# Kernel optimization log

Measured on AMD Instinct MI355X. Metric: run time of the kernel, lower is better.

## Reference

```python
import jax, jax.numpy as jnp
import numpy as np

L, H, C, V, BLK = 6, 16, 1024, 32000, 2048
B, T, TA = 2, 512, 512
DFF = 4 * C
STD = 0.02
PROJ_STD = 0.02 / np.sqrt(2 * L)  # c_proj init per module
SCALE = 1.0 / np.sqrt(C // H)


def setup_inputs() -> dict:
    key = jax.random.key(0)
    ks = iter(jax.random.split(key, 64))
    nrm = lambda shape, std=STD: jax.random.normal(next(ks), shape, jnp.float32) * std
    inp = {
        'idx': jax.random.randint(next(ks), (B, T), 0, V),
        'xa': jax.random.normal(next(ks), (B, TA, C), jnp.float32),
        'wte': nrm((V, C)),            # tied with lm_head
        'wpe': nrm((BLK, C)),
        'ln1_w': jnp.ones((L, C)), 'ln1_b': jnp.zeros((L, C)),
        'sa_wq': nrm((L, C, C)), 'sa_bq': jnp.zeros((L, C)),
        'sa_wk': nrm((L, C, C)), 'sa_bk': jnp.zeros((L, C)),
        'sa_wv': nrm((L, C, C)), 'sa_bv': jnp.zeros((L, C)),
        'sa_wo': nrm((L, C, C), PROJ_STD), 'sa_bo': jnp.zeros((L, C)),
        'ca_wq': nrm((L, C, C)), 'ca_bq': jnp.zeros((L, C)),
        'ca_wk': nrm((L, C, C)), 'ca_bk': jnp.zeros((L, C)),
        'ca_wv': nrm((L, C, C)), 'ca_bv': jnp.zeros((L, C)),
        'ca_wo': nrm((L, C, C), PROJ_STD), 'ca_bo': jnp.zeros((L, C)),
        'ln2_w': jnp.ones((L, C)), 'ln2_b': jnp.zeros((L, C)),
        'fc_w': nrm((L, C, DFF)), 'fc_b': jnp.zeros((L, DFF)),
        'pr_w': nrm((L, DFF, C), PROJ_STD), 'pr_b': jnp.zeros((L, C)),
        'lnf_w': jnp.ones((C,)), 'lnf_b': jnp.zeros((C,)),
    }
    return inp


def _ln(h, w, b):
    m = h.mean(-1, keepdims=True)
    v = jnp.mean((h - m) ** 2, -1, keepdims=True)
    return (h - m) * jax.lax.rsqrt(v + 1e-5) * w + b


def _gelu(h):  # new_gelu (tanh approximation)
    return 0.5 * h * (1.0 + jnp.tanh(np.sqrt(2.0 / np.pi) * (h + 0.044715 * h ** 3)))


def _attn(hq, hkv, wq, bq, wk, bk, wv, bv, wo, bo):
    # NB: the original applies a tril causal mask even for cross-attention.
    Bq, Tq, _ = hq.shape
    Tk = hkv.shape[1]
    D = C // H
    q = (hq @ wq + bq).reshape(Bq, Tq, H, D)
    k = (hkv @ wk + bk).reshape(Bq, Tk, H, D)
    v = (hkv @ wv + bv).reshape(Bq, Tk, H, D)
    att = jnp.einsum('bqhd,bkhd->bhqk', q, k) * SCALE
    mask = jnp.tril(jnp.ones((Tq, Tk), bool))
    att = jnp.where(mask, att, -jnp.inf)
    att = jax.nn.softmax(att, axis=-1)
    y = jnp.einsum('bhqk,bkhd->bqhd', att, v).reshape(Bq, Tq, C)
    return y @ wo + bo


def _forward(idx, xa, wte, wpe, ln1_w, ln1_b, sa_wq, sa_bq, sa_wk, sa_bk, sa_wv, sa_bv, sa_wo, sa_bo,
             ca_wq, ca_bq, ca_wk, ca_bk, ca_wv, ca_bv, ca_wo, ca_bo,
             ln2_w, ln2_b, fc_w, fc_b, pr_w, pr_b, lnf_w, lnf_b):
    t = idx.shape[1]
    x = wte[idx] + wpe[:t][None]  # [B,T,C]

    def block(h, p):
        (l1w, l1b, sqw, sqb, skw, skb, svw, svb, sow, sob,
         cqw, cqb, ckw, ckb, cvw, cvb, cow, cob,
         l2w, l2b, fw, fb, pw, pb) = p
        n = _ln(h, l1w, l1b)
        h = h + _attn(n, n, sqw, sqb, skw, skb, svw, svb, sow, sob)
        n = _ln(h, l1w, l1b)  # ln_1 reused for cross-attn, as in source
        h = h + _attn(n, xa, cqw, cqb, ckw, ckb, cvw, cvb, cow, cob)
        n = _ln(h, l2w, l2b)
        h = h + (_gelu(n @ fw + fb) @ pw + pb)
        return h, None

    xs = (ln1_w, ln1_b, sa_wq, sa_bq, sa_wk, sa_bk, sa_wv, sa_bv, sa_wo, sa_bo,
          ca_wq, ca_bq, ca_wk, ca_bk, ca_wv, ca_bv, ca_wo, ca_bo,
          ln2_w, ln2_b, fc_w, fc_b, pr_w, pr_b)
    x, _ = jax.lax.scan(block, x, xs)
    x = _ln(x, lnf_w, lnf_b)
    return x @ wte.T  # tied lm_head, [B,T,V]


def reference(idx, xa, wte, wpe, ln1_w, ln1_b, sa_wq, sa_bq, sa_wk, sa_bk, sa_wv, sa_bv, sa_wo, sa_bo,
              ca_wq, ca_bq, ca_wk, ca_bk, ca_wv, ca_bv, ca_wo, ca_bo,
              ln2_w, ln2_b, fc_w, fc_b, pr_w, pr_b, lnf_w, lnf_b):
    return _forward(idx, xa, wte, wpe, ln1_w, ln1_b, sa_wq, sa_bq, sa_wk, sa_bk, sa_wv, sa_bv, sa_wo, sa_bo,
                    ca_wq, ca_bq, ca_wk, ca_bk, ca_wv, ca_bv, ca_wo, ca_bo,
                    ln2_w, ln2_b, fc_w, fc_b, pr_w, pr_b, lnf_w, lnf_b)
```

## Files before the change

### kernel.cpp

```cpp
#include <hip/hip_runtime.h>
#include <math.h>

#define CC   1024
#define HH   16
#define DH   64
#define TT   512
#define NTOK 1024
#define DFF_ 4096
#define VV   32000
#define QKSCALE 0.125f

typedef unsigned short u16;
typedef __attribute__((ext_vector_type(8))) short short8;
typedef __attribute__((ext_vector_type(4))) float f32x4;

__device__ __forceinline__ u16 f2bf(float f) {
  union { float f; unsigned u; } v; v.f = f;
  unsigned r = v.u + 0x7FFFu + ((v.u >> 16) & 1u);
  return (u16)(r >> 16);
}
__device__ __forceinline__ float gelu_f(float h) {
  return 0.5f * h * (1.0f + tanhf(0.7978845608028654f * (h + 0.044715f * h * h * h)));
}

#define GLD16(gp, lp) __builtin_amdgcn_global_load_lds( \
    (const __attribute__((address_space(1))) void*)(gp), \
    (__attribute__((address_space(3))) void*)(lp), 16, 0, 0)

#define MFMA(a, b, c) __builtin_amdgcn_mfma_f32_16x16x32_bf16(a, b, c, 0, 0, 0)

__global__ __launch_bounds__(256) void embed_kernel(
    const int* __restrict__ idx, const float* __restrict__ wte,
    const float* __restrict__ wpe, float* __restrict__ x) {
  int row = blockIdx.x;
  int t = row & (TT - 1);
  int id = idx[row];
  const float4* a = (const float4*)(wte + (size_t)id * CC);
  const float4* p = (const float4*)(wpe + (size_t)t * CC);
  float4* o = (float4*)(x + (size_t)row * CC);
  int c = threadIdx.x;
  float4 va = a[c], vp = p[c];
  float4 ov;
  ov.x = va.x + vp.x; ov.y = va.y + vp.y; ov.z = va.z + vp.z; ov.w = va.w + vp.w;
  o[c] = ov;
}

__global__ __launch_bounds__(256) void ln_kernel(
    const float* __restrict__ x, const float* __restrict__ w,
    const float* __restrict__ b, u16* __restrict__ out) {
  int row = blockIdx.x, tid = threadIdx.x;
  float4 v = ((const float4*)(x + (size_t)row * CC))[tid];
  float s  = v.x + v.y + v.z + v.w;
  float sq = fmaf(v.x, v.x, fmaf(v.y, v.y, fmaf(v.z, v.z, v.w * v.w)));
  for (int o = 32; o > 0; o >>= 1) { s += __shfl_down(s, o); sq += __shfl_down(sq, o); }
  __shared__ float rs[4], rq[4];
  int wid = tid >> 6, lane = tid & 63;
  if (lane == 0) { rs[wid] = s; rq[wid] = sq; }
  __syncthreads();
  s  = rs[0] + rs[1] + rs[2] + rs[3];
  sq = rq[0] + rq[1] + rq[2] + rq[3];
  float mean = s * (1.0f / CC);
  float var  = sq * (1.0f / CC) - mean * mean;
  float rstd = 1.0f / sqrtf(var + 1e-5f);
  float4 wv = ((const float4*)w)[tid];
  float4 bv = ((const float4*)b)[tid];
  ushort4 o;
  o.x = f2bf((v.x - mean) * rstd * wv.x + bv.x);
  o.y = f2bf((v.y - mean) * rstd * wv.y + bv.y);
  o.z = f2bf((v.z - mean) * rstd * wv.z + bv.z);
  o.w = f2bf((v.w - mean) * rstd * wv.w + bv.w);
  ((ushort4*)(out + (size_t)row * CC))[tid] = o;
}

__global__ __launch_bounds__(256) void wtransL_kernel(
    const float* __restrict__ w0, const float* __restrict__ w1,
    const float* __restrict__ w2, const float* __restrict__ w3,
    const float* __restrict__ w4, const float* __restrict__ w5,
    const float* __restrict__ w6, const float* __restrict__ w7,
    const float* __restrict__ fc, const float* __restrict__ pr,
    u16* __restrict__ wt, size_t dls, int lbase) {
  const size_t M1 = 1048576;
  int z = blockIdx.z;
  int l = lbase + (z >> 4), slot = z & 15;
  size_t wofs = (size_t)l * M1;
  size_t mofs = (size_t)l * 4 * M1;
  const float* src;
  size_t doff = (size_t)(l - lbase) * dls;
  int sstr, dstr;
  if (slot < 8) {
    const float* base = slot == 0 ? w0 : slot == 1 ? w1 : slot == 2 ? w2
                      : slot == 3 ? w3 : slot == 4 ? w4 : slot == 5 ? w5
                      : slot == 6 ? w6 : w7;
    src = base + wofs; sstr = 1024; doff += (size_t)slot * M1; dstr = 1024;
  } else if (slot < 12) {
    int s = slot - 8;
    src = fc + mofs + (size_t)s * 1024; sstr = 4096;
    doff += 8 * M1 + (size_t)s * M1; dstr = 1024;
  } else {
    int s = slot - 12;
    src = pr + mofs + (size_t)s * M1; sstr = 1024;
    doff += 12 * M1 + (size_t)s * 1024; dstr = 4096;
  }
  __shared__ float t[32][33];
  int bx = blockIdx.x * 32, by = blockIdx.y * 32;
  int c = threadIdx.x & 31, r = threadIdx.x >> 5;
#pragma unroll
  for (int i = 0; i < 4; ++i)
    t[r + i * 8][c] = src[(size_t)(by + r + i * 8) * sstr + bx + c];
  __syncthreads();
#pragma unroll
  for (int i = 0; i < 4; ++i)
    wt[doff + (size_t)(bx + r + i * 8) * dstr + by + c] = f2bf(t[c][r + i * 8]);
}

__global__ __launch_bounds__(256) void convbf_kernel(
    const float* __restrict__ in, u16* __restrict__ out, int n4) {
  int i = blockIdx.x * 256 + threadIdx.x;
  if (i < n4) {
    float4 v = ((const float4*)in)[i];
    ushort4 o; o.x = f2bf(v.x); o.y = f2bf(v.y); o.z = f2bf(v.z); o.w = f2bf(v.w);
    ((ushort4*)out)[i] = o;
  }
}

template <int EPI, int MODE, int BM, int BN, int BK>
__global__ __launch_bounds__(256) void gemm_bf16_kernel(
    const u16* __restrict__ A, const u16* __restrict__ A2,
    const u16* __restrict__ B, const u16* __restrict__ B2,
    const float* __restrict__ bias, const float* __restrict__ bias2,
    const float* __restrict__ bias3, float* __restrict__ Cm,
    int K, int ldc, int whichbase) {
  constexpr int WM = BM / 2, WN = BN / 2, MF = WM / 16, NF = WN / 16;
  constexpr int KS = BK / 32;
  constexpr int NB = BK / 8;
  constexpr int PA = BM * BK / 2048;
  constexpr int PB = BN * BK / 2048;
  constexpr int RPP = 2048 / BK;
  __shared__ u16 As[2][BM * BK];
  __shared__ u16 Bs[2][BN * BK];
  int tid = threadIdx.x;
  int lane = tid & 63, wave = tid >> 6;
  int wr = wave >> 1, wc = wave & 1;
  int row0, col0;
  bool isq = true;
  const u16* Ause = A;
  const u16* Buse = B;
  if (MODE == 2) {
    int id = blockIdx.x;
    int wg = (id & 7) * 250 + (id >> 3);
    row0 = (wg & 7) * BM;
    col0 = (wg >> 3) * BN;
  } else if (MODE == 3) {
    int bx = blockIdx.x;
    isq = bx < (1024 / BN);
    Ause = isq ? A : A2;
    Buse = isq ? B : B2;
    col0 = (isq ? bx : bx - 1024 / BN) * BN;
    row0 = blockIdx.y * BM;
  } else {
    row0 = blockIdx.y * BM;
    col0 = blockIdx.x * BN;
  }
  f32x4 acc[MF][NF];
#pragma unroll
  for (int m = 0; m < MF; ++m)
#pragma unroll
    for (int n = 0; n < NF; ++n) acc[m][n] = (f32x4){0.f, 0.f, 0.f, 0.f};

  int srow = tid / NB;
  int sblk = (BK == 64) ? ((tid & 7) ^ ((tid >> 3) & 7))
                        : ((tid & 3) ^ ((tid >> 3) & 3));
  const u16* Ab = Ause + (size_t)row0 * K;
  int arow = wr * WM + (lane & 15);
  int brow = wc * WN + (lane & 15);
  int g8 = lane >> 4;
  const int NT = K / BK;

  auto compute = [&](const u16* Ac, const u16* Bc) {
#pragma unroll
    for (int ks = 0; ks < KS; ++ks) {
      short8 af[MF], bg[NF];
#pragma unroll
      for (int m = 0; m < MF; ++m) {
        int row = arow + m * 16;
        int off = (BK == 64) ? row * 64 + (((ks * 4 + g8) ^ (row & 7)) << 3)
                             : row * 32 + ((g8 ^ ((row >> 1) & 3)) << 3);
        af[m] = *(const short8*)&Ac[off];
      }
#pragma unroll
      for (int n = 0; n < NF; ++n) {
        int row = brow + n * 16;
        int off = (BK == 64) ? row * 64 + (((ks * 4 + g8) ^ (row & 7)) << 3)
                             : row * 32 + ((g8 ^ ((row >> 1) & 3)) << 3);
        bg[n] = *(const short8*)&Bc[off];
      }
      __builtin_amdgcn_s_setprio(1);
#pragma unroll
      for (int m = 0; m < MF; ++m)
#pragma unroll
        for (int n = 0; n < NF; ++n)
          acc[m][n] = MFMA(af[m], bg[n], acc[m][n]);
      __builtin_amdgcn_s_setprio(0);
    }
  };

  if constexpr (MODE == 2) {
    const float* Bf = (const float*)B;
    int bsr = tid >> 2;
    int bkb = tid & 3;
    float4 rb0, rb1, rb2, rb3;
    auto loadB = [&](int k0) {
      const float* p0 = Bf + (size_t)(col0 + bsr) * 1024 + k0 + bkb * 8;
      const float* p1 = Bf + (size_t)(col0 + 64 + bsr) * 1024 + k0 + bkb * 8;
      rb0 = *(const float4*)p0; rb1 = *(const float4*)(p0 + 4);
      rb2 = *(const float4*)p1; rb3 = *(const float4*)(p1 + 4);
    };
    auto writeB = [&](int bufi) {
      u16 t0[8] = {f2bf(rb0.x), f2bf(rb0.y), f2bf(rb0.z), f2bf(rb0.w),
                   f2bf(rb1.x), f2bf(rb1.y), f2bf(rb1.z), f2bf(rb1.w)};
      u16 t1[8] = {f2bf(rb2.x), f2bf(rb2.y), f2bf(rb2.z), f2bf(rb2.w),
                   f2bf(rb3.x), f2bf(rb3.y), f2bf(rb3.z), f2bf(rb3.w)};
      int r1 = 64 + bsr;
      *(short8*)&Bs[bufi][bsr * 32 + ((bkb ^ ((bsr >> 1) & 3)) << 3)] = *(short8*)t0;
      *(short8*)&Bs[bufi][r1 * 32 + ((bkb ^ ((r1 >> 1) & 3)) << 3)] = *(short8*)t1;
    };
    auto stageA = [&](int bufi, int k0) {
#pragma unroll
      for (int p = 0; p < PA; ++p)
        GLD16(Ab + (size_t)(p * RPP + srow) * K + k0 + sblk * 8,
              &As[bufi][p * 2048 + wave * 512]);
    };
    loadB(0);
    stageA(0, 0);
    writeB(0);
    __syncthreads();
    for (int t = 0; t < NT; ++t) {
      int cur = t & 1;
      if (t + 1 < NT) { loadB((t + 1) * BK); stageA(cur ^ 1, (t + 1) * BK); }
      compute(As[cur], Bs[cur]);
      if (t + 1 < NT) writeB(cur ^ 1);
      __syncthreads();
    }
  } else {
    const u16* Bb = Buse + (size_t)col0 * K;
    auto stage = [&](int bufi, int k0) {
#pragma unroll
      for (int p = 0; p < PA; ++p)
        GLD16(Ab + (size_t)(p * RPP + srow) * K + k0 + sblk * 8,
              &As[bufi][p * 2048 + wave * 512]);
#pragma unroll
      for (int p = 0; p < PB; ++p)
        GLD16(Bb + (size_t)(p * RPP + srow) * K + k0 + sblk * 8,
              &Bs[bufi][p * 2048 + wave * 512]);
    };
    stage(0, 0);
    __syncthreads();
    for (int t = 0; t < NT; ++t) {
      int cur = t & 1;
      if (t + 1 < NT) stage(cur ^ 1, (t + 1) * BK);
      compute(As[cur], Bs[cur]);
      __syncthreads();
    }
  }

  int r0 = row0 + wr * WM + g8 * 4;
  int c0 = col0 + wc * WN + (lane & 15);

  if (EPI == 4) {
    u16* qb = (u16*)Cm;
#pragma unroll
    for (int m = 0; m < MF; ++m)
#pragma unroll
      for (int n = 0; n < NF; ++n) {
        int j = c0 + n * 16;
        int which = (MODE == 3 ? (isq ? 0 : 1) : whichbase) + (j >> 10);
        const float* bp = which == 0 ? bias : (which == 1 ? bias2 : bias3);
        float bj = bp ? bp[j & 1023] : 0.0f;
        int h = (j & 1023) >> 6, d = j & 63;
        int trow0 = r0 + m * 16;
        int b = trow0 >> 9, t0 = trow0 & 511;
        int bh = b * 16 + h;
        u16 vals[4];
#pragma unroll
        for (int r = 0; r < 4; ++r) vals[r] = f2bf(acc[m][n][r] + bj);
        if (which < 2) {
          u16* dst = qb + (size_t)which * 1048576 + (size_t)bh * 32768 + (size_t)t0 * 64 + d;
#pragma unroll
          for (int r = 0; r < 4; ++r) dst[(size_t)r * 64] = vals[r];
        } else {
          u16* dst = qb + 2 * 1048576 + (size_t)bh * 32768 + (size_t)d * 512 + t0;
          *(ushort4*)dst = *(ushort4*)vals;
        }
      }
    return;
  }

  float bj[NF];
#pragma unroll
  for (int n = 0; n < NF; ++n)
    bj[n] = bias ? bias[c0 + n * 16] : 0.0f;
  u16* Cb = (u16*)Cm;
#pragma unroll
  for (int m = 0; m < MF; ++m)
#pragma unroll
    for (int n = 0; n < NF; ++n)
#pragma unroll
      for (int r = 0; r < 4; ++r) {
        size_t off = (size_t)(r0 + m * 16 + r) * ldc + c0 + n * 16;
        float v = acc[m][n][r] + bj[n];
        if (EPI == 0) Cm[off] = v;
        else if (EPI == 1) Cm[off] += v;
        else if (EPI == 2) Cb[off] = f2bf(gelu_f(v));
      }
}

__global__ __launch_bounds__(256) void attn_kernel(
    const u16* __restrict__ qh, const u16* __restrict__ kh,
    const u16* __restrict__ vt, u16* __restrict__ y) {
  __shared__ u16 P[32 * 512];
  __shared__ float smax[4][32], ssum[4][32];
  int tid = threadIdx.x, lane = tid & 63, w = tid >> 6;
  int bx = blockIdx.x, bh = blockIdx.y;
  int q0 = bx * 32;
  int b = bh >> 4, h = bh & 15;
  const u16* qb = qh + (size_t)bh * 32768;
  const u16* kb = kh + (size_t)bh * 32768;
  const u16* vb = vt + (size_t)bh * 32768;
  int g = lane >> 4, c = lane & 15;

  short8 a[2][2];
#pragma unroll
  for (int rt = 0; rt < 2; ++rt)
#pragma unroll
    for (int ks = 0; ks < 2; ++ks)
      a[rt][ks] = *(const short8*)(qb + (size_t)(q0 + rt * 16 + c) * 64 + ks * 32 + g * 8);

  int lim = q0 + 31;
  int nct = (lim - w * 128) / 16 + 1;
  if (nct > 8) nct = 8;
  if (nct < 0) nct = 0;
  f32x4 s[2][8];
#pragma unroll
  for (int rt = 0; rt < 2; ++rt)
#pragma unroll
    for (int ct = 0; ct < 8; ++ct) s[rt][ct] = (f32x4){0.f, 0.f, 0.f, 0.f};
  for (int ct = 0; ct < nct; ++ct) {
    int n0 = w * 128 + ct * 16;
#pragma unroll
    for (int ks = 0; ks < 2; ++ks) {
      short8 bf = *(const short8*)(kb + (size_t)(n0 + c) * 64 + ks * 32 + g * 8);
      s[0][ct] = MFMA(a[0][ks], bf, s[0][ct]);
      s[1][ct] = MFMA(a[1][ks], bf, s[1][ct]);
    }
  }

  float mx[2][4];
#pragma unroll
  for (int rt = 0; rt < 2; ++rt)
#pragma unroll
    for (int r = 0; r < 4; ++r) mx[rt][r] = -1e30f;
  for (int ct = 0; ct < nct; ++ct) {
    int col = w * 128 + ct * 16 + c;
#pragma unroll
    for (int rt = 0; rt < 2; ++rt)
#pragma unroll
      for (int r = 0; r < 4; ++r) {
        int trow = q0 + rt * 16 + g * 4 + r;
        float v = s[rt][ct][r] * QKSCALE;
        if (col > trow) v = -1e30f;
        s[rt][ct][r] = v;
        mx[rt][r] = fmaxf(mx[rt][r], v);
      }
  }
#pragma unroll
  for (int off = 1; off < 16; off <<= 1)
#pragma unroll
    for (int rt = 0; rt < 2; ++rt)
#pragma unroll
      for (int r = 0; r < 4; ++r) mx[rt][r] = fmaxf(mx[rt][r], __shfl_xor(mx[rt][r], off));
  if (c == 0)
#pragma unroll
    for (int rt = 0; rt < 2; ++rt)
#pragma unroll
      for (int r = 0; r < 4; ++r) smax[w][rt * 16 + g * 4 + r] = mx[rt][r];
  __syncthreads();

  float m_[2][4], sum[2][4];
#pragma unroll
  for (int rt = 0; rt < 2; ++rt)
#pragma unroll
    for (int r = 0; r < 4; ++r) {
      int row = rt * 16 + g * 4 + r;
      m_[rt][r] = fmaxf(fmaxf(smax[0][row], smax[1][row]), fmaxf(smax[2][row], smax[3][row]));
      sum[rt][r] = 0.f;
    }
  for (int ct = 0; ct < nct; ++ct) {
    int col = w * 128 + ct * 16 + c;
    int blk = col >> 3, cl = col & 7;
#pragma unroll
    for (int rt = 0; rt < 2; ++rt)
#pragma unroll
      for (int r = 0; r < 4; ++r) {
        float p = __expf(s[rt][ct][r] - m_[rt][r]);
        sum[rt][r] += p;
        int row = rt * 16 + g * 4 + r;
        int hsh = (row ^ (row >> 2)) & 7;
        P[row * 512 + ((blk ^ hsh) << 3) + cl] = f2bf(p);
      }
  }
#pragma unroll
  for (int off = 1; off < 16; off <<= 1)
#pragma unroll
    for (int rt = 0; rt < 2; ++rt)
#pragma unroll
      for (int r = 0; r < 4; ++r) sum[rt][r] += __shfl_xor(sum[rt][r], off);
  if (c == 0)
#pragma unroll
    for (int rt = 0; rt < 2; ++rt)
#pragma unroll
      for (int r = 0; r < 4; ++r) ssum[w][rt * 16 + g * 4 + r] = sum[rt][r];
  __syncthreads();

  float li[2][4];
#pragma unroll
  for (int rt = 0; rt < 2; ++rt)
#pragma unroll
    for (int r = 0; r < 4; ++r) {
      int row = rt * 16 + g * 4 + r;
      li[rt][r] = 1.0f / (ssum[0][row] + ssum[1][row] + ssum[2][row] + ssum[3][row]);
    }

  int rt2 = w >> 1, nh = w & 1;
  f32x4 o[2];
  o[0] = (f32x4){0.f, 0.f, 0.f, 0.f};
  o[1] = (f32x4){0.f, 0.f, 0.f, 0.f};
  int nks = bx + 1;
  int prow = rt2 * 16 + c;
  int phsh = (prow ^ (prow >> 2)) & 7;
  for (int ks = 0; ks < nks; ++ks) {
    short8 pa = *(const short8*)&P[prow * 512 + (((ks * 4 + g) ^ phsh) << 3)];
#pragma unroll
    for (int nt = 0; nt < 2; ++nt) {
      int d = nh * 32 + nt * 16 + c;
      short8 vf = *(const short8*)(vb + (size_t)d * 512 + ks * 32 + g * 8);
      o[nt] = MFMA(pa, vf, o[nt]);
    }
  }
#pragma unroll
  for (int nt = 0; nt < 2; ++nt)
#pragma unroll
    for (int r = 0; r < 4; ++r) {
      int trow = q0 + rt2 * 16 + g * 4 + r;
      float val = o[nt][r] * li[rt2][r];
      y[(size_t)(b * 512 + trow) * 1024 + h * 64 + nh * 32 + nt * 16 + c] = f2bf(val);
    }
}

extern "C" void kernel_launch(void* const* d_in, const int* in_sizes, int n_in,
                              void* d_out, int out_size, void* d_ws, size_t ws_size,
                              hipStream_t stream) {
  const int*   idx   = (const int*)d_in[0];
  const float* xa    = (const float*)d_in[1];
  const float* wte   = (const float*)d_in[2];
  const float* wpe   = (const float*)d_in[3];
  const float* ln1_w = (const float*)d_in[4];
  const float* ln1_b = (const float*)d_in[5];
  const float* sa_wq = (const float*)d_in[6];
  const float* sa_bq = (const float*)d_in[7];
  const float* sa_wk = (const float*)d_in[8];
  const float* sa_bk = (const float*)d_in[9];
  const float* sa_wv = (const float*)d_in[10];
  const float* sa_bv = (const float*)d_in[11];
  const float* sa_wo = (const float*)d_in[12];
  const float* sa_bo = (const float*)d_in[13];
  const float* ca_wq = (const float*)d_in[14];
  const float* ca_bq = (const float*)d_in[15];
  const float* ca_wk = (const float*)d_in[16];
  const float* ca_bk = (const float*)d_in[17];
  const float* ca_wv = (const float*)d_in[18];
  const float* ca_bv = (const float*)d_in[19];
  const float* ca_wo = (const float*)d_in[20];
  const float* ca_bo = (const float*)d_in[21];
  const float* ln2_w = (const float*)d_in[22];
  const float* ln2_b = (const float*)d_in[23];
  const float* fc_w  = (const float*)d_in[24];
  const float* fc_b  = (const float*)d_in[25];
  const float* pr_w  = (const float*)d_in[26];
  const float* pr_b  = (const float*)d_in[27];
  const float* lnf_w = (const float*)d_in[28];
  const float* lnf_b = (const float*)d_in[29];

  const size_t M1 = 1048576;
  float* ws     = (float*)d_ws;
  float* x      = ws;
  u16* qkvh  = (u16*)(x + M1);
  u16* nbf   = qkvh + 3 * M1;
  u16* ybf   = nbf + M1;
  u16* hmbf  = ybf + M1;
  u16* xabf  = hmbf + 4 * M1;
  u16* wT    = xabf + M1;

  const bool full = ws_size >= 226492416ull;
  const size_t wls = full ? 16 * M1 : 0;

  const size_t oQKV = 0, oWO = 3 * M1, oCQ = 4 * M1, oCKV = 5 * M1,
               oCWO = 7 * M1, oFC = 8 * M1, oPR = 12 * M1;

  embed_kernel<<<NTOK, 256, 0, stream>>>(idx, wte, wpe, x);
  convbf_kernel<<<(NTOK * CC / 4 + 255) / 256, 256, 0, stream>>>(xa, xabf, NTOK * CC / 4);
  if (full)
    wtransL_kernel<<<dim3(32, 32, 96), 256, 0, stream>>>(
        sa_wq, sa_wk, sa_wv, sa_wo, ca_wq, ca_wk, ca_wv, ca_wo,
        fc_w, pr_w, wT, wls, 0);

  for (int l = 0; l < 6; ++l) {
    size_t bofs = (size_t)l * CC;
    u16* wTl = wT + (size_t)l * wls;

    if (!full)
      wtransL_kernel<<<dim3(32, 32, 16), 256, 0, stream>>>(
          sa_wq, sa_wk, sa_wv, sa_wo, ca_wq, ca_wk, ca_wv, ca_wo,
          fc_w, pr_w, wT, 0, l);

    ln_kernel<<<NTOK, 256, 0, stream>>>(x, ln1_w + bofs, ln1_b + bofs, nbf);
    gemm_bf16_kernel<4, 0, 64, 128, 64><<<dim3(24, 16), 256, 0, stream>>>(
        nbf, nullptr, wTl + oQKV, nullptr, sa_bq + bofs, sa_bk + bofs,
        sa_bv + bofs, (float*)qkvh, CC, 0, 0);
    attn_kernel<<<dim3(16, 32), 256, 0, stream>>>(qkvh, qkvh + M1, qkvh + 2 * M1, ybf);
    gemm_bf16_kernel<1, 0, 32, 64, 64><<<dim3(16, 32), 256, 0, stream>>>(
        ybf, nullptr, wTl + oWO, nullptr, sa_bo + bofs, nullptr, nullptr,
        x, CC, CC, 0);

    ln_kernel<<<NTOK, 256, 0, stream>>>(x, ln1_w + bofs, ln1_b + bofs, nbf);
    gemm_bf16_kernel<4, 3, 64, 64, 64><<<dim3(48, 16), 256, 0, stream>>>(
        nbf, xabf, wTl + oCQ, wTl + oCKV, ca_bq + bofs, ca_bk + bofs,
        ca_bv + bofs, (float*)qkvh, CC, 0, 0);
    attn_kernel<<<dim3(16, 32), 256, 0, stream>>>(qkvh, qkvh + M1, qkvh + 2 * M1, ybf);
    gemm_bf16_kernel<1, 0, 32, 64, 64><<<dim3(16, 32), 256, 0, stream>>>(
        ybf, nullptr, wTl + oCWO, nullptr, ca_bo + bofs, nullptr, nullptr,
        x, CC, CC, 0);

    ln_kernel<<<NTOK, 256, 0, stream>>>(x, ln2_w + bofs, ln2_b + bofs, nbf);
    gemm_bf16_kernel<2, 0, 64, 128, 64><<<dim3(32, 16), 256, 0, stream>>>(
        nbf, nullptr, wTl + oFC, nullptr, fc_b + (size_t)l * DFF_, nullptr,
        nullptr, (float*)hmbf, CC, DFF_, 0);
    gemm_bf16_kernel<1, 0, 32, 64, 64><<<dim3(16, 32), 256, 0, stream>>>(
        hmbf, nullptr, wTl + oPR, nullptr, pr_b + bofs, nullptr, nullptr,
        x, DFF_, CC, 0);
  }

  ln_kernel<<<NTOK, 256, 0, stream>>>(x, lnf_w, lnf_b, nbf);
  gemm_bf16_kernel<0, 2, 128, 128, 32><<<dim3(2000), 256, 0, stream>>>(
      nbf, nullptr, (const u16*)wte, nullptr, nullptr, nullptr, nullptr,
      (float*)d_out, CC, VV, 0);
}
```

Before: 1.649 ms.

## Split-K residual GEMMs with atomic accumulation and vectorize weight transpose

Adds a split-K template parameter to the bf16 GEMM. The three residual-add projections (two attention output projections and the MLP down projection) now launch 2 or 4 K-splits that accumulate into x with atomicAdd, and only the first split adds the bias. This raises the block count for these narrow 1024-column GEMMs to improve CU occupancy, at the cost of atomic traffic and a nondeterministic summation order. The weight transpose kernel also moves to 64x64 tiles with float4 loads and ushort4 stores to cut per-element memory transactions.

New measurement: 1.521 ms. 1.08x faster.

```diff
diff --git a/kernel.cpp b/kernel.cpp
--- a/kernel.cpp
+++ b/kernel.cpp
@@ -101,16 +101,28 @@
     src = pr + mofs + (size_t)s * M1; sstr = 1024;
     doff += 12 * M1 + (size_t)s * 1024; dstr = 4096;
   }
-  __shared__ float t[32][33];
-  int bx = blockIdx.x * 32, by = blockIdx.y * 32;
-  int c = threadIdx.x & 31, r = threadIdx.x >> 5;
-#pragma unroll
-  for (int i = 0; i < 4; ++i)
-    t[r + i * 8][c] = src[(size_t)(by + r + i * 8) * sstr + bx + c];
+  __shared__ float t[64][65];
+  int bx = blockIdx.x * 64, by = blockIdx.y * 64;
+  int tid = threadIdx.x;
+  int r16 = tid >> 4;
+  int c4  = (tid & 15) * 4;
+#pragma unroll
+  for (int i = 0; i < 4; ++i) {
+    int row = r16 + i * 16;
+    float4 v = *(const float4*)&src[(size_t)(by + row) * sstr + bx + c4];
+    t[row][c4] = v.x; t[row][c4 + 1] = v.y; t[row][c4 + 2] = v.z; t[row][c4 + 3] = v.w;
+  }
   __syncthreads();
 #pragma unroll
-  for (int i = 0; i < 4; ++i)
-    wt[doff + (size_t)(bx + r + i * 8) * dstr + by + c] = f2bf(t[c][r + i * 8]);
+  for (int i = 0; i < 4; ++i) {
+    int orow = r16 + i * 16;
+    ushort4 o;
+    o.x = f2bf(t[c4 + 0][orow]);
+    o.y = f2bf(t[c4 + 1][orow]);
+    o.z = f2bf(t[c4 + 2][orow]);
+    o.w = f2bf(t[c4 + 3][orow]);
+    *(ushort4*)&wt[doff + (size_t)(bx + orow) * dstr + by + c4] = o;
+  }
 }
 
 __global__ __launch_bounds__(256) void convbf_kernel(
@@ -123,7 +135,7 @@
   }
 }
 
-template <int EPI, int MODE, int BM, int BN, int BK>
+template <int EPI, int MODE, int BM, int BN, int BK, int SK>
 __global__ __launch_bounds__(256) void gemm_bf16_kernel(
     const u16* __restrict__ A, const u16* __restrict__ A2,
     const u16* __restrict__ B, const u16* __restrict__ B2,
@@ -161,6 +173,9 @@
     row0 = blockIdx.y * BM;
     col0 = blockIdx.x * BN;
   }
+  const int split = (SK > 1) ? blockIdx.z : 0;
+  const int Kloc = K / SK;
+  const int kbase = split * Kloc;
   f32x4 acc[MF][NF];
 #pragma unroll
   for (int m = 0; m < MF; ++m)
@@ -170,11 +185,11 @@
   int srow = tid / NB;
   int sblk = (BK == 64) ? ((tid & 7) ^ ((tid >> 3) & 7))
                         : ((tid & 3) ^ ((tid >> 3) & 3));
-  const u16* Ab = Ause + (size_t)row0 * K;
+  const u16* Ab = Ause + (size_t)row0 * K + kbase;
   int arow = wr * WM + (lane & 15);
   int brow = wc * WN + (lane & 15);
   int g8 = lane >> 4;
-  const int NT = K / BK;
+  const int NT = Kloc / BK;
 
   auto compute = [&](const u16* Ac, const u16* Bc) {
 #pragma unroll
@@ -242,7 +257,7 @@
       __syncthreads();
     }
   } else {
-    const u16* Bb = Buse + (size_t)col0 * K;
+    const u16* Bb = Buse + (size_t)col0 * K + kbase;
     auto stage = [&](int bufi, int k0) {
 #pragma unroll
       for (int p = 0; p < PA; ++p)
@@ -307,9 +322,12 @@
 #pragma unroll
       for (int r = 0; r < 4; ++r) {
         size_t off = (size_t)(r0 + m * 16 + r) * ldc + c0 + n * 16;
-        float v = acc[m][n][r] + bj[n];
+        float v = acc[m][n][r] + ((SK == 1 || split == 0) ? bj[n] : 0.0f);
         if (EPI == 0) Cm[off] = v;
-        else if (EPI == 1) Cm[off] += v;
+        else if (EPI == 1) {
+          if constexpr (SK > 1) atomicAdd(&Cm[off], v);
+          else Cm[off] += v;
+        }
         else if (EPI == 2) Cb[off] = f2bf(gelu_f(v));
       }
 }
@@ -509,7 +527,7 @@
   embed_kernel<<<NTOK, 256, 0, stream>>>(idx, wte, wpe, x);
   convbf_kernel<<<(NTOK * CC / 4 + 255) / 256, 256, 0, stream>>>(xa, xabf, NTOK * CC / 4);
   if (full)
-    wtransL_kernel<<<dim3(32, 32, 96), 256, 0, stream>>>(
+    wtransL_kernel<<<dim3(16, 16, 96), 256, 0, stream>>>(
         sa_wq, sa_wk, sa_wv, sa_wo, ca_wq, ca_wk, ca_wv, ca_wo,
         fc_w, pr_w, wT, wls, 0);
 
@@ -518,39 +536,39 @@
     u16* wTl = wT + (size_t)l * wls;
 
     if (!full)
-      wtransL_kernel<<<dim3(32, 32, 16), 256, 0, stream>>>(
+      wtransL_kernel<<<dim3(16, 16, 16), 256, 0, stream>>>(
           sa_wq, sa_wk, sa_wv, sa_wo, ca_wq, ca_wk, ca_wv, ca_wo,
           fc_w, pr_w, wT, 0, l);
 
     ln_kernel<<<NTOK, 256, 0, stream>>>(x, ln1_w + bofs, ln1_b + bofs, nbf);
-    gemm_bf16_kernel<4, 0, 64, 128, 64><<<dim3(24, 16), 256, 0, stream>>>(
+    gemm_bf16_kernel<4, 0, 64, 128, 64, 1><<<dim3(24, 16), 256, 0, stream>>>(
         nbf, nullptr, wTl + oQKV, nullptr, sa_bq + bofs, sa_bk + bofs,
         sa_bv + bofs, (float*)qkvh, CC, 0, 0);
     attn_kernel<<<dim3(16, 32), 256, 0, stream>>>(qkvh, qkvh + M1, qkvh + 2 * M1, ybf);
-    gemm_bf16_kernel<1, 0, 32, 64, 64><<<dim3(16, 32), 256, 0, stream>>>(
+    gemm_bf16_kernel<1, 0, 32, 64, 64, 2><<<dim3(16, 32, 2), 256, 0, stream>>>(
         ybf, nullptr, wTl + oWO, nullptr, sa_bo + bofs, nullptr, nullptr,
         x, CC, CC, 0);
 
     ln_kernel<<<NTOK, 256, 0, stream>>>(x, ln1_w + bofs, ln1_b + bofs, nbf);
-    gemm_bf16_kernel<4, 3, 64, 64, 64><<<dim3(48, 16), 256, 0, stream>>>(
+    gemm_bf16_kernel<4, 3, 64, 64, 64, 1><<<dim3(48, 16), 256, 0, stream>>>(
         nbf, xabf, wTl + oCQ, wTl + oCKV, ca_bq + bofs, ca_bk + bofs,
         ca_bv + bofs, (float*)qkvh, CC, 0, 0);
     attn_kernel<<<dim3(16, 32), 256, 0, stream>>>(qkvh, qkvh + M1, qkvh + 2 * M1, ybf);
-    gemm_bf16_kernel<1, 0, 32, 64, 64><<<dim3(16, 32), 256, 0, stream>>>(
+    gemm_bf16_kernel<1, 0, 32, 64, 64, 2><<<dim3(16, 32, 2), 256, 0, stream>>>(
         ybf, nullptr, wTl + oCWO, nullptr, ca_bo + bofs, nullptr, nullptr,
         x, CC, CC, 0);
 
     ln_kernel<<<NTOK, 256, 0, stream>>>(x, ln2_w + bofs, ln2_b + bofs, nbf);
-    gemm_bf16_kernel<2, 0, 64, 128, 64><<<dim3(32, 16), 256, 0, stream>>>(
+    gemm_bf16_kernel<2, 0, 64, 128, 64, 1><<<dim3(32, 16), 256, 0, stream>>>(
         nbf, nullptr, wTl + oFC, nullptr, fc_b + (size_t)l * DFF_, nullptr,
         nullptr, (float*)hmbf, CC, DFF_, 0);
-    gemm_bf16_kernel<1, 0, 32, 64, 64><<<dim3(16, 32), 256, 0, stream>>>(
+    gemm_bf16_kernel<1, 0, 32, 64, 64, 4><<<dim3(16, 32, 4), 256, 0, stream>>>(
         hmbf, nullptr, wTl + oPR, nullptr, pr_b + bofs, nullptr, nullptr,
         x, DFF_, CC, 0);
   }
 
   ln_kernel<<<NTOK, 256, 0, stream>>>(x, lnf_w, lnf_b, nbf);
-  gemm_bf16_kernel<0, 2, 128, 128, 32><<<dim3(2000), 256, 0, stream>>>(
+  gemm_bf16_kernel<0, 2, 128, 128, 32, 1><<<dim3(2000), 256, 0, stream>>>(
       nbf, nullptr, (const u16*)wte, nullptr, nullptr, nullptr, nullptr,
       (float*)d_out, CC, VV, 0);
 }
```
